# Optimization experiments

Hardware: AMD Instinct MI355X
Metric: run time of the kernel (lower is better)

Reference implementation:

```python
import jax, jax.numpy as jnp
import numpy as np

DEPTH = 6
N_LEAVES = 2 ** DEPTH


def setup_inputs() -> dict:
    key = jax.random.key(0)
    ks = jax.random.split(key, 7)
    in_f, lw, out_f = 1024, 64, 512
    B = 4096
    s1 = 1.0 / np.sqrt(in_f)
    s2 = 1.0 / np.sqrt(lw)
    return {
        "x": jax.random.normal(ks[0], (B, in_f), jnp.float32),
        "node_weights": jax.random.uniform(ks[1], (N_LEAVES - 1, in_f), jnp.float32, -s1, s1),
        "node_biases": jax.random.uniform(ks[2], (N_LEAVES - 1, 1), jnp.float32, -s1, s1),
        "w1s": jax.random.uniform(ks[3], (N_LEAVES, in_f, lw), jnp.float32, -s1, s1),
        "b1s": jax.random.uniform(ks[4], (N_LEAVES, lw), jnp.float32, -s1, s1),
        "w2s": jax.random.uniform(ks[5], (N_LEAVES, lw, out_f), jnp.float32, -s2, s2),
        "b2s": jax.random.uniform(ks[6], (N_LEAVES, out_f), jnp.float32, -s2, s2),
    }


def _fff_forward(x, node_weights, node_biases, w1s, b1s, w2s, b2s):
    B = x.shape[0]
    # Soft routing: build per-leaf mixture weights level by level (training path).
    mixture = jnp.ones((B, N_LEAVES), x.dtype)
    for d in range(DEPTH):
        platform = 2 ** d - 1
        n_nodes = 2 ** d
        w = node_weights[platform:platform + n_nodes]          # (n, in)
        b = node_biases[platform:platform + n_nodes]            # (n, 1)
        logits = x @ w.T + b.T                                  # (B, n)
        be = jax.nn.sigmoid(logits)
        mod = jnp.stack([1.0 - be, be], axis=-1).reshape(B, 2 * n_nodes)
        mixture = (mixture.reshape(B, 2 * n_nodes, N_LEAVES // (2 * n_nodes))
                   * mod[:, :, None]).reshape(B, N_LEAVES)
    # All-leaf expert MLPs (grouped GEMMs), then mixture-weighted sum.
    h = jax.nn.relu(jnp.einsum('bi,liw->blw', x, w1s) + b1s[None])   # (B, L, W)
    y = jnp.einsum('blw,lwo->blo', h, w2s) + b2s[None]                # (B, L, O)
    return jnp.sum(y * mixture[:, :, None], axis=1)                   # (B, O)


def reference(x, node_weights, node_biases, w1s, b1s, w2s, b2s):
    return _fff_forward(x, node_weights, node_biases, w1s, b1s, w2s, b2s)
```

## Files before the change

### kernel.cpp

```cpp
#include <hip/hip_runtime.h>
#include <hip/hip_bf16.h>

typedef unsigned short u16;
typedef __attribute__((ext_vector_type(8))) short bf16x8;
typedef __attribute__((ext_vector_type(4))) float f32x4;
typedef __attribute__((ext_vector_type(16))) float f32x16;
typedef __attribute__((ext_vector_type(4))) unsigned short u16x4;
typedef __attribute__((ext_vector_type(8))) unsigned short u16x8;

#define BATCH 4096
#define INF   1024
#define NH    4096
#define OUTF  512
#define NLEAF 64
#define FDEPTH 6
#define ZSPL  4

__device__ __align__(16) u16  g_Xb[(size_t)BATCH * INF];
__device__ __align__(16) u16  g_W1t[(size_t)NH * INF];
__device__ __align__(16) u16  g_W2t[(size_t)OUTF * NH];
__device__ __align__(16) u16  g_NWh[(size_t)64 * INF];
__device__ __align__(16) u16  g_B2t[(size_t)OUTF * 64];
__device__ __align__(16) u16  g_Hb[(size_t)BATCH * NH];
__device__ __align__(16) float g_mix[(size_t)BATCH * NLEAF];
__device__ __align__(16) float g_part[(size_t)ZSPL * BATCH * OUTF];

__device__ inline u16 f2b(float f) {
  __hip_bfloat16 h = __float2bfloat16(f);
  return *reinterpret_cast<u16*>(&h);
}

__device__ inline void async16(const u16* g, u16* l) {
  __builtin_amdgcn_global_load_lds((const __attribute__((address_space(1))) void*)g,
                                   (__attribute__((address_space(3))) void*)l, 16, 0, 0);
}

__global__ __launch_bounds__(256) void prep_kernel(
    const float* __restrict__ x, const float* __restrict__ nw,
    const float* __restrict__ w1s, const float* __restrict__ w2s,
    const float* __restrict__ b2s) {
  __shared__ float tile[64 * 65];
  const int b = blockIdx.x;
  const int t = threadIdx.x;

  if (b < 2048) {
    int i = (b * 256 + t) * 8;
    float4 v0 = *(const float4*)(x + i);
    float4 v1 = *(const float4*)(x + i + 4);
    u16x8 h;
    h[0] = f2b(v0.x); h[1] = f2b(v0.y); h[2] = f2b(v0.z); h[3] = f2b(v0.w);
    h[4] = f2b(v1.x); h[5] = f2b(v1.y); h[6] = f2b(v1.z); h[7] = f2b(v1.w);
    *(u16x8*)(g_Xb + i) = h;
    return;
  }
  if (b < 2112) {
    int idx = ((b - 2048) * 256 + t) * 4;
    int n = idx >> 10;
    float4 v = make_float4(0.f, 0.f, 0.f, 0.f);
    if (n < 63) v = *(const float4*)(nw + idx);
    u16x4 h;
    h[0] = f2b(v.x); h[1] = f2b(v.y); h[2] = f2b(v.z); h[3] = f2b(v.w);
    *(u16x4*)(g_NWh + idx) = h;
    return;
  }

  const float* sb;
  u16* db;
  int R, C, r0, c0;
  if (b < 3136) {
    int idx = b - 2112;
    int z = idx >> 4;
    R = 1024; C = 64;
    r0 = (idx & 15) * 64; c0 = 0;
    sb = w1s + (size_t)z * R * C;
    db = g_W1t + (size_t)z * R * C;
  } else if (b < 3648) {
    int idx = b - 3136;
    R = 4096; C = 512;
    r0 = (idx >> 3) * 64; c0 = (idx & 7) * 64;
    sb = w2s;
    db = g_W2t;
  } else {
    int idx = b - 3648;
    R = 64; C = 512;
    r0 = 0; c0 = idx * 64;
    sb = b2s;
    db = g_B2t;
  }
  int cc4 = (t & 15) * 4;
#pragma unroll
  for (int it = 0; it < 4; ++it) {
    int rr = (t >> 4) + it * 16;
    float4 v = *(const float4*)(sb + (size_t)(r0 + rr) * C + c0 + cc4);
    tile[rr * 65 + cc4 + 0] = v.x;
    tile[rr * 65 + cc4 + 1] = v.y;
    tile[rr * 65 + cc4 + 2] = v.z;
    tile[rr * 65 + cc4 + 3] = v.w;
  }
  __syncthreads();
  int cc = t >> 2, rch = (t & 3) * 16;
  u16x8 o0, o1;
#pragma unroll
  for (int j = 0; j < 8; ++j) o0[j] = f2b(tile[(rch + j) * 65 + cc]);
#pragma unroll
  for (int j = 0; j < 8; ++j) o1[j] = f2b(tile[(rch + 8 + j) * 65 + cc]);
  u16* p = db + (size_t)(c0 + cc) * R + r0 + rch;
  *(u16x8*)p = o0;
  *(u16x8*)(p + 8) = o1;
}

__global__ __launch_bounds__(256) void mixture_kernel(
    const float* __restrict__ nb, float* __restrict__ out) {
  __shared__ __align__(16) unsigned char lds[57344];
  const int t = threadIdx.x;
  const int wv = t >> 6, ln = t & 63;
  const int quad = ln >> 4, m16 = ln & 15;
  const int r0 = blockIdx.x * 16;

  u16* stW = (u16*)(lds + wv * 10240);
  u16* stX = (u16*)(lds + wv * 10240 + 8192);
  float* lred = (float*)lds;
  float* ssig = (float*)(lds + 16384);
  u16* smixb = (u16*)(lds + 20480);
  u16* b2l = (u16*)(lds + 24576);

  f32x4 acc[4] = {};
#pragma unroll 1
  for (int it = 0; it < 4; ++it) {
    int kc = wv * 256 + it * 64;
#pragma unroll
    for (int j = 0; j < 8; ++j) {
      int id = j * 64 + ln;
      int row = id >> 3, c8 = (id & 7) ^ (row & 7);
      async16(g_NWh + (size_t)row * INF + kc + c8 * 8, stW + j * 512);
    }
#pragma unroll
    for (int j = 0; j < 2; ++j) {
      int id = j * 64 + ln;
      int row = id >> 3, c8 = (id & 7) ^ (row & 7);
      async16(g_Xb + (size_t)(r0 + row) * INF + kc + c8 * 8, stX + j * 512);
    }
    __syncthreads();
#pragma unroll
    for (int ks = 0; ks < 2; ++ks) {
      bf16x8 bF = *(const bf16x8*)(stX + m16 * 64 + ((ks * 4 + quad) ^ (m16 & 7)) * 8);
#pragma unroll
      for (int tw = 0; tw < 4; ++tw) {
        int row = tw * 16 + m16;
        bf16x8 aF = *(const bf16x8*)(stW + row * 64 + ((ks * 4 + quad) ^ (row & 7)) * 8);
        acc[tw] = __builtin_amdgcn_mfma_f32_16x16x32_bf16(aF, bF, acc[tw], 0, 0, 0);
      }
    }
    __syncthreads();
  }
#pragma unroll
  for (int tw = 0; tw < 4; ++tw)
#pragma unroll
    for (int r = 0; r < 4; ++r)
      lred[((size_t)wv * 64 + tw * 16 + quad * 4 + r) * 16 + m16] = acc[tw][r];
  __syncthreads();

#pragma unroll
  for (int j = 0; j < 8; ++j) {
    int id = (wv * 8 + j) * 64 + ln;
    int row = id >> 3, c8 = (id & 7) ^ (row & 7);
    async16(g_B2t + (size_t)row * 64 + c8 * 8, b2l + (wv * 8 + j) * 512);
  }

  {
    int n = t & 63, rg = t >> 6;
#pragma unroll
    for (int rr = 0; rr < 4; ++rr) {
      int row = rg * 4 + rr;
      float s = lred[(0 * 64 + n) * 16 + row] + lred[(1 * 64 + n) * 16 + row] +
                lred[(2 * 64 + n) * 16 + row] + lred[(3 * 64 + n) * 16 + row];
      if (n < 63) s += nb[n];
      ssig[row * 64 + n] = 1.f / (1.f + __expf(-s));
    }
  }
  __syncthreads();
  {
    int leaf = t & 63, rg = t >> 6;
#pragma unroll
    for (int rr = 0; rr < 4; ++rr) {
      int row = rg * 4 + rr;
      float p = 1.f;
#pragma unroll
      for (int d = 0; d < FDEPTH; ++d) {
        int node = (1 << d) - 1 + (leaf >> (FDEPTH - d));
        int bit = (leaf >> (FDEPTH - 1 - d)) & 1;
        float s = ssig[row * 64 + node];
        p *= bit ? s : (1.f - s);
      }
      g_mix[(size_t)(r0 + row) * 64 + leaf] = p;
      smixb[row * 64 + ((leaf >> 3) ^ (row & 7)) * 8 + (leaf & 7)] = f2b(p);
    }
  }
  __syncthreads();

  bf16x8 mixF[2];
#pragma unroll
  for (int ks = 0; ks < 2; ++ks)
    mixF[ks] = *(const bf16x8*)(smixb + m16 * 64 + ((ks * 4 + quad) ^ (m16 & 7)) * 8);
#pragma unroll 1
  for (int s = 0; s < 2; ++s) {
    f32x4 sacc[4] = {};
#pragma unroll
    for (int tile = 0; tile < 4; ++tile) {
#pragma unroll
      for (int ks = 0; ks < 2; ++ks) {
        int lrow = wv * 64 + tile * 16 + m16;
        bf16x8 aF = *(const bf16x8*)(b2l + lrow * 64 + ((ks * 4 + quad) ^ (lrow & 7)) * 8);
        sacc[tile] = __builtin_amdgcn_mfma_f32_16x16x32_bf16(aF, mixF[ks], sacc[tile], 0, 0, 0);
      }
    }
#pragma unroll
    for (int tile = 0; tile < 4; ++tile) {
      int o = s * 256 + wv * 64 + tile * 16 + quad * 4;
      *(f32x4*)(out + (size_t)(r0 + m16) * OUTF + o) = sacc[tile];
    }
    if (s == 0) {
      __syncthreads();
#pragma unroll
      for (int j = 0; j < 8; ++j) {
        int id = (wv * 8 + j) * 64 + ln;
        int row = id >> 3, c8 = (id & 7) ^ (row & 7);
        async16(g_B2t + (size_t)(256 + row) * 64 + c8 * 8, b2l + (wv * 8 + j) * 512);
      }
      __syncthreads();
    }
  }
}

__global__ __launch_bounds__(256) void gemm1_kernel(const float* __restrict__ b1) {
  constexpr int BM = 128, BN = 128, BK = 64, K = 1024, LD = 1024;

  __shared__ u16 lsA[BM * BK];
  __shared__ u16 lsB[BN * BK];

  const int t = threadIdx.x;
  const int wv = t >> 6, ln = t & 63;
  const int wm = wv >> 1, wn = wv & 1;
  const int l32 = ln & 31, lh = ln >> 5;
  const int am0 = blockIdx.y * BM;
  const int bn0 = blockIdx.x * BN;

  f32x16 acc[2][2] = {};

  for (int kc = 0; kc < K; kc += BK) {
#pragma unroll
    for (int i = 0; i < 4; ++i) {
      int id = i * 256 + t;
      int row = id >> 3;
      int c8 = (id & 7) ^ (row & 7);
      async16(g_Xb + (size_t)(am0 + row) * LD + kc + c8 * 8, lsA + (i * 256 + wv * 64) * 8);
    }
#pragma unroll
    for (int i = 0; i < 4; ++i) {
      int id = i * 256 + t;
      int row = id >> 3;
      int c8 = (id & 7) ^ (row & 7);
      async16(g_W1t + (size_t)(bn0 + row) * LD + kc + c8 * 8, lsB + (i * 256 + wv * 64) * 8);
    }
    __syncthreads();
#pragma unroll
    for (int ks = 0; ks < 4; ++ks) {
      bf16x8 wF[2], xF[2];
#pragma unroll
      for (int tw = 0; tw < 2; ++tw) {
        int row = wn * 64 + tw * 32 + l32;
        wF[tw] = *(const bf16x8*)(lsB + row * BK + ((ks * 2 + lh) ^ (row & 7)) * 8);
      }
#pragma unroll
      for (int tb = 0; tb < 2; ++tb) {
        int row = wm * 64 + tb * 32 + l32;
        xF[tb] = *(const bf16x8*)(lsA + row * BK + ((ks * 2 + lh) ^ (row & 7)) * 8);
      }
#pragma unroll
      for (int tw = 0; tw < 2; ++tw)
#pragma unroll
        for (int tb = 0; tb < 2; ++tb)
          acc[tw][tb] = __builtin_amdgcn_mfma_f32_32x32x16_bf16(wF[tw], xF[tb], acc[tw][tb], 0, 0, 0);
    }
    __syncthreads();
  }

  const int leaf = (bn0 >> 6) + wn;
#pragma unroll
  for (int tb = 0; tb < 2; ++tb) {
    int bg = am0 + wm * 64 + tb * 32 + l32;
    float mixv = g_mix[(size_t)bg * 64 + leaf];
#pragma unroll
    for (int tw = 0; tw < 2; ++tw) {
#pragma unroll
      for (int g = 0; g < 4; ++g) {
        int col0 = bn0 + wn * 64 + tw * 32 + g * 8 + lh * 4;
        float4 b1v = *(const float4*)(b1 + col0);
        u16x4 pk;
        pk[0] = f2b(fmaxf(acc[tw][tb][g * 4 + 0] + b1v.x, 0.f) * mixv);
        pk[1] = f2b(fmaxf(acc[tw][tb][g * 4 + 1] + b1v.y, 0.f) * mixv);
        pk[2] = f2b(fmaxf(acc[tw][tb][g * 4 + 2] + b1v.z, 0.f) * mixv);
        pk[3] = f2b(fmaxf(acc[tw][tb][g * 4 + 3] + b1v.w, 0.f) * mixv);
        *(u16x4*)(g_Hb + (size_t)bg * NH + col0) = pk;
      }
    }
  }
}

__global__ __launch_bounds__(256) void gemm2_kernel() {
  constexpr int BM = 128, BN = 128, BK = 64, K = 4096, LD = 4096;

  __shared__ u16 lsA[BM * BK];
  __shared__ u16 lsB[BN * BK];

  const int bid = blockIdx.x;
  const int xcd = bid & 7, slot = bid >> 3;
  const int ytile = xcd * 4 + (slot >> 4);
  const int rem = slot & 15;
  const int xtile = rem & 3, zidx = rem >> 2;

  const int t = threadIdx.x;
  const int wv = t >> 6, ln = t & 63;
  const int wm = wv >> 1, wn = wv & 1;
  const int quad = ln >> 4, m16 = ln & 15;
  const int am0 = ytile * BM;
  const int bn0 = xtile * BN;
  const int kbeg = zidx * (K / ZSPL);
  const int kend = kbeg + K / ZSPL;

  f32x4 acc[4][4] = {};

  for (int kc = kbeg; kc < kend; kc += BK) {
#pragma unroll
    for (int i = 0; i < 4; ++i) {
      int id = i * 256 + t;
      int row = id >> 3;
      int c8 = (id & 7) ^ (row & 7);
      async16(g_Hb + (size_t)(am0 + row) * LD + kc + c8 * 8, lsA + (i * 256 + wv * 64) * 8);
    }
#pragma unroll
    for (int i = 0; i < 4; ++i) {
      int id = i * 256 + t;
      int row = id >> 3;
      int c8 = (id & 7) ^ (row & 7);
      async16(g_W2t + (size_t)(bn0 + row) * LD + kc + c8 * 8, lsB + (i * 256 + wv * 64) * 8);
    }
    __syncthreads();
#pragma unroll
    for (int ks = 0; ks < 2; ++ks) {
      bf16x8 wF[4], xF[4];
#pragma unroll
      for (int tw = 0; tw < 4; ++tw) {
        int row = wn * 64 + tw * 16 + m16;
        wF[tw] = *(const bf16x8*)(lsB + row * BK + ((ks * 4 + quad) ^ (row & 7)) * 8);
      }
#pragma unroll
      for (int tb = 0; tb < 4; ++tb) {
        int row = wm * 64 + tb * 16 + m16;
        xF[tb] = *(const bf16x8*)(lsA + row * BK + ((ks * 4 + quad) ^ (row & 7)) * 8);
      }
#pragma unroll
      for (int tw = 0; tw < 4; ++tw)
#pragma unroll
        for (int tb = 0; tb < 4; ++tb)
          acc[tw][tb] = __builtin_amdgcn_mfma_f32_16x16x32_bf16(wF[tw], xF[tb], acc[tw][tb], 0, 0, 0);
    }
    __syncthreads();
  }

  float* part = g_part + (size_t)zidx * ((size_t)BATCH * OUTF);
#pragma unroll
  for (int tw = 0; tw < 4; ++tw) {
    int og = bn0 + wn * 64 + tw * 16 + quad * 4;
#pragma unroll
    for (int tb = 0; tb < 4; ++tb) {
      int bg = am0 + wm * 64 + tb * 16 + m16;
      *(f32x4*)(part + (size_t)bg * OUTF + og) = acc[tw][tb];
    }
  }
}

__global__ __launch_bounds__(256) void reduce_kernel(float* __restrict__ out) {
  int i = (blockIdx.x * 256 + threadIdx.x) * 4;
  float4 s = *(const float4*)(out + i);
#pragma unroll
  for (int z = 0; z < ZSPL; ++z) {
    const float4 p = *(const float4*)(g_part + (size_t)z * BATCH * OUTF + i);
    s.x += p.x; s.y += p.y; s.z += p.z; s.w += p.w;
  }
  *(float4*)(out + i) = s;
}

extern "C" void kernel_launch(void* const* d_in, const int* in_sizes, int n_in,
                              void* d_out, int out_size, void* d_ws, size_t ws_size,
                              hipStream_t stream) {
  const float* x = (const float*)d_in[0];
  const float* nw = (const float*)d_in[1];
  const float* nb = (const float*)d_in[2];
  const float* w1s = (const float*)d_in[3];
  const float* b1s = (const float*)d_in[4];
  const float* w2s = (const float*)d_in[5];
  const float* b2s = (const float*)d_in[6];
  float* out = (float*)d_out;
  (void)d_ws; (void)ws_size;

  hipLaunchKernelGGL(prep_kernel, dim3(3656), dim3(256), 0, stream,
                     x, nw, w1s, w2s, b2s);
  hipLaunchKernelGGL(mixture_kernel, dim3(256), dim3(256), 0, stream, nb, out);
  hipLaunchKernelGGL(gemm1_kernel, dim3(32, 32), dim3(256), 0, stream, b1s);
  hipLaunchKernelGGL(gemm2_kernel, dim3(512), dim3(256), 0, stream);
  hipLaunchKernelGGL(reduce_kernel, dim3(2048), dim3(256), 0, stream, out);
}
```

Baseline: 203.6 us.

## Fuse split-K reduction into gemm2 and linearize gemm1 LDS fragment layout

The separate reduce kernel is removed. Each gemm2 block writes its split-K partial, then increments a per-tile atomic counter, and the last block to arrive sums the four partials into the output. The counters are reset inside prep_kernel. Gemm1 now stores its tiles in LDS in MFMA-fragment order, so each wave reads a contiguous block without XOR swizzling, and the X and W1 async loads are merged into one loop. The cost is less coalesced global loads in gemm1 (32-byte row segments) and serialized tail work in the last-arriving gemm2 blocks.

```diff
diff --git a/kernel.cpp b/kernel.cpp
--- a/kernel.cpp
+++ b/kernel.cpp
@@ -24,6 +24,7 @@
 __device__ __align__(16) u16  g_Hb[(size_t)BATCH * NH];
 __device__ __align__(16) float g_mix[(size_t)BATCH * NLEAF];
 __device__ __align__(16) float g_part[(size_t)ZSPL * BATCH * OUTF];
+__device__ int g_scnt[128];
 
 __device__ inline u16 f2b(float f) {
   __hip_bfloat16 h = __float2bfloat16(f);
@@ -86,6 +87,7 @@
     r0 = 0; c0 = idx * 64;
     sb = b2s;
     db = g_B2t;
+    if (t < 16) g_scnt[idx * 16 + t] = 0;
   }
   int cc4 = (t & 15) * 4;
 #pragma unroll
@@ -250,32 +252,22 @@
   for (int kc = 0; kc < K; kc += BK) {
 #pragma unroll
     for (int i = 0; i < 4; ++i) {
-      int id = i * 256 + t;
-      int row = id >> 3;
-      int c8 = (id & 7) ^ (row & 7);
-      async16(g_Xb + (size_t)(am0 + row) * LD + kc + c8 * 8, lsA + (i * 256 + wv * 64) * 8);
-    }
-#pragma unroll
-    for (int i = 0; i < 4; ++i) {
-      int id = i * 256 + t;
-      int row = id >> 3;
-      int c8 = (id & 7) ^ (row & 7);
-      async16(g_W1t + (size_t)(bn0 + row) * LD + kc + c8 * 8, lsB + (i * 256 + wv * 64) * 8);
+      int row = i * 32 + l32;
+      int c8 = wv * 2 + lh;
+      const size_t goff = (size_t)row * LD + kc + c8 * 8;
+      async16(g_Xb + (size_t)am0 * LD + goff, lsA + (i * 256 + wv * 64) * 8);
+      async16(g_W1t + (size_t)bn0 * LD + goff, lsB + (i * 256 + wv * 64) * 8);
     }
     __syncthreads();
 #pragma unroll
     for (int ks = 0; ks < 4; ++ks) {
       bf16x8 wF[2], xF[2];
 #pragma unroll
-      for (int tw = 0; tw < 2; ++tw) {
-        int row = wn * 64 + tw * 32 + l32;
-        wF[tw] = *(const bf16x8*)(lsB + row * BK + ((ks * 2 + lh) ^ (row & 7)) * 8);
-      }
-#pragma unroll
-      for (int tb = 0; tb < 2; ++tb) {
-        int row = wm * 64 + tb * 32 + l32;
-        xF[tb] = *(const bf16x8*)(lsA + row * BK + ((ks * 2 + lh) ^ (row & 7)) * 8);
-      }
+      for (int tw = 0; tw < 2; ++tw)
+        wF[tw] = *(const bf16x8*)(lsB + (wn * 2 + tw) * 2048 + ks * 512 + ln * 8);
+#pragma unroll
+      for (int tb = 0; tb < 2; ++tb)
+        xF[tb] = *(const bf16x8*)(lsA + (wm * 2 + tb) * 2048 + ks * 512 + ln * 8);
 #pragma unroll
       for (int tw = 0; tw < 2; ++tw)
 #pragma unroll
@@ -307,7 +299,7 @@
   }
 }
 
-__global__ __launch_bounds__(256) void gemm2_kernel() {
+__global__ __launch_bounds__(256) void gemm2_kernel(float* __restrict__ out) {
   constexpr int BM = 128, BN = 128, BK = 64, K = 4096, LD = 4096;
 
   __shared__ u16 lsA[BM * BK];
@@ -368,27 +360,43 @@
     __syncthreads();
   }
 
-  float* part = g_part + (size_t)zidx * ((size_t)BATCH * OUTF);
-#pragma unroll
-  for (int tw = 0; tw < 4; ++tw) {
-    int og = bn0 + wn * 64 + tw * 16 + quad * 4;
-#pragma unroll
-    for (int tb = 0; tb < 4; ++tb) {
-      int bg = am0 + wm * 64 + tb * 16 + m16;
-      *(f32x4*)(part + (size_t)bg * OUTF + og) = acc[tw][tb];
-    }
-  }
-}
-
-__global__ __launch_bounds__(256) void reduce_kernel(float* __restrict__ out) {
-  int i = (blockIdx.x * 256 + threadIdx.x) * 4;
-  float4 s = *(const float4*)(out + i);
-#pragma unroll
-  for (int z = 0; z < ZSPL; ++z) {
-    const float4 p = *(const float4*)(g_part + (size_t)z * BATCH * OUTF + i);
-    s.x += p.x; s.y += p.y; s.z += p.z; s.w += p.w;
-  }
-  *(float4*)(out + i) = s;
+  {
+    float* part = g_part + (size_t)zidx * ((size_t)BATCH * OUTF);
+#pragma unroll
+    for (int tw = 0; tw < 4; ++tw) {
+      int og = bn0 + wn * 64 + tw * 16 + quad * 4;
+#pragma unroll
+      for (int tb = 0; tb < 4; ++tb) {
+        int bg = am0 + wm * 64 + tb * 16 + m16;
+        *(f32x4*)(part + (size_t)bg * OUTF + og) = acc[tw][tb];
+      }
+    }
+  }
+
+  __threadfence();
+  __shared__ int swin;
+  if (t == 0) {
+    int old = atomicAdd(&g_scnt[ytile * 4 + xtile], 1);
+    swin = (old == ZSPL - 1) ? 1 : 0;
+  }
+  __syncthreads();
+  if (swin) {
+    __threadfence();
+    const size_t base = (size_t)am0 * OUTF + bn0;
+#pragma unroll
+    for (int c = 0; c < 16; ++c) {
+      int idx = (c * 256 + t) * 4;
+      int row = idx >> 7, col = idx & 127;
+      size_t off = base + (size_t)row * OUTF + col;
+      float4 s = *(const float4*)(out + off);
+#pragma unroll
+      for (int z = 0; z < ZSPL; ++z) {
+        const float4 p = *(const float4*)(g_part + (size_t)z * BATCH * OUTF + off);
+        s.x += p.x; s.y += p.y; s.z += p.z; s.w += p.w;
+      }
+      *(float4*)(out + off) = s;
+    }
+  }
 }
 
 extern "C" void kernel_launch(void* const* d_in, const int* in_sizes, int n_in,
@@ -408,6 +416,5 @@
                      x, nw, w1s, w2s, b2s);
   hipLaunchKernelGGL(mixture_kernel, dim3(256), dim3(256), 0, stream, nb, out);
   hipLaunchKernelGGL(gemm1_kernel, dim3(32, 32), dim3(256), 0, stream, b1s);
-  hipLaunchKernelGGL(gemm2_kernel, dim3(512), dim3(256), 0, stream);
-  hipLaunchKernelGGL(reduce_kernel, dim3(2048), dim3(256), 0, stream, out);
-}
+  hipLaunchKernelGGL(gemm2_kernel, dim3(512), dim3(256), 0, stream, out);
+}
```

New measurement: 327.5 us. 60.9% more time.
